# Performance work log

Measured on AMD Instinct MI355X. Metric: run time of the kernel, lower is better.

The kernel has to match this reference:

```python
import jax, jax.numpy as jnp
import numpy as np

H = 8
D_MODEL = 512
D_K = D_MODEL // H
B = 8
S = 1024


def _linear(x, W, b):
    # torch nn.Linear: y = x @ W.T + b, W: [out, in]
    return jnp.einsum('bsd,ed->bse', x, W) + b


def _to_heads(x):
    # [B,S,D] -> [B,H,S,d_k]
    return x.reshape(B, S, H, D_K).transpose(0, 2, 1, 3)


def setup_inputs() -> dict:
    key = jax.random.key(0)
    ks = jax.random.split(key, 20)
    inp = {
        'input_rgb': jax.random.normal(ks[0], (B, S, D_MODEL), jnp.float32),
        'input_flow': jax.random.normal(ks[1], (B, S, D_MODEL), jnp.float32),
    }
    names = ['Wq1', 'Wk1', 'Wv1', 'Wq2', 'Wk2', 'Wv2', 'Wo1', 'Wo2']
    for i, n in enumerate(names):
        inp[n] = jax.random.normal(ks[2 + i], (D_MODEL, D_MODEL), jnp.float32) * 0.02
        inp['b' + n[1:]] = jax.random.normal(ks[10 + i], (D_MODEL,), jnp.float32) * 0.02
    return inp


def reference(input_rgb, input_flow, Wq1, bq1, Wk1, bk1, Wv1, bv1,
              Wq2, bq2, Wk2, bk2, Wv2, bv2, Wo1, bo1, Wo2, bo2):
    scale = 1.0 / jnp.sqrt(jnp.asarray(D_K, input_rgb.dtype))

    q_r = _to_heads(_linear(input_rgb, Wq1, bq1))
    k_r = _to_heads(_linear(input_rgb, Wk1, bk1))
    v_r = _to_heads(_linear(input_rgb, Wv1, bv1))
    q_f = _to_heads(_linear(input_flow, Wq2, bq2))
    k_f = _to_heads(_linear(input_flow, Wk2, bk2))
    v_f = _to_heads(_linear(input_flow, Wv2, bv2))

    # two full [B,H,S,S] softmax attention maps
    attn_rgb = jax.nn.softmax(jnp.einsum('bhqd,bhkd->bhqk', q_r, k_r) * scale, axis=-1)
    attn_flow = jax.nn.softmax(jnp.einsum('bhqd,bhkd->bhqk', q_f, k_f) * scale, axis=-1)
    # elementwise max merge (breaks flash-attention fusion)
    attn = jnp.maximum(attn_rgb, attn_flow)

    # Attention2: out = attn @ value (dropout is identity in eval mode)
    out_rgb = jnp.einsum('bhqk,bhkd->bhqd', attn, v_r)
    out_flow = jnp.einsum('bhqk,bhkd->bhqd', attn, v_f)

    out_rgb = out_rgb.transpose(0, 2, 1, 3).reshape(B, S, D_MODEL)
    out_flow = out_flow.transpose(0, 2, 1, 3).reshape(B, S, D_MODEL)
    return (_linear(out_rgb, Wo1, bo1), _linear(out_flow, Wo2, bo2))
```

## Files before the change

kernel.cpp:

```cpp
#include <hip/hip_runtime.h>
#include <hip/hip_bf16.h>


typedef unsigned short u16;
typedef __attribute__((ext_vector_type(8))) short short8;
typedef __attribute__((ext_vector_type(4))) short s4pack;
typedef __attribute__((ext_vector_type(4))) float floatx4;

#define B_DIM 8
#define S_DIM 1024
#define H_DIM 8
#define DK 64
#define DMODEL 512
#define NTOK (B_DIM * S_DIM)
#define SEG ((size_t)NTOK * DMODEL)
#define WSEG ((size_t)DMODEL * DMODEL)

#define SCHED_FENCE() __builtin_amdgcn_sched_barrier(0)
#define LGKM0() asm volatile("s_waitcnt lgkmcnt(0)" ::: "memory")
#define VMCNT0() asm volatile("s_waitcnt vmcnt(0)" ::: "memory")
#define BARRIER() __builtin_amdgcn_s_barrier()

__device__ __forceinline__ floatx4 mfma_bf16(short8 a, short8 b, floatx4 c) {
  return __builtin_amdgcn_mfma_f32_16x16x32_bf16(a, b, c, 0, 0, 0);
}

__device__ __forceinline__ void mfma16(floatx4& c, s4pack a, s4pack b) {
  asm volatile("v_mfma_f32_16x16x16_bf16 %0, %1, %2, %0"
               : "+v"(c) : "v"(a), "v"(b));
}

__device__ __forceinline__ u16 f32_to_bf16_rne(float f) {
  unsigned u = __float_as_uint(f);
  unsigned r = u + 0x7FFFu + ((u >> 16) & 1u);
  return (u16)(r >> 16);
}

__device__ __forceinline__ float bf16_bits_to_f32(u16 u) {
  return __uint_as_float(((unsigned)u) << 16);
}

__device__ __forceinline__ void async_cp16(const u16* g, u16* lds) {
  __builtin_amdgcn_global_load_lds(
      (__attribute__((address_space(1))) void*)(const_cast<u16*>(g)),
      (__attribute__((address_space(3))) void*)(lds), 16, 0, 0);
}

#define NT_CONV 18
struct ConvParams {
  const void* src[NT_CONV];
  u16* dst[NT_CONV];
  int n[NT_CONV];
  int coff[NT_CONV + 1];
};

__global__ __launch_bounds__(256) void convert_inputs(ConvParams p) {
  __shared__ int flag_f32;
  const int blk = blockIdx.x;
  int t = 0;
  while (t + 1 < NT_CONV && blk >= p.coff[t + 1]) ++t;
  const int lc = blk - p.coff[t];
  const int n = p.n[t];
  const int tid = threadIdx.x;

  if (tid < 64) {
    const u16* s = (const u16*)p.src[t];
    int bad = 0;
#pragma unroll
    for (int j = 0; j < 8; ++j) {
      float f = bf16_bits_to_f32(s[tid * 8 + j]);
      bad |= !(fabsf(f) < 1e4f);
    }
    bad |= __shfl_xor(bad, 1);
    bad |= __shfl_xor(bad, 2);
    bad |= __shfl_xor(bad, 4);
    bad |= __shfl_xor(bad, 8);
    bad |= __shfl_xor(bad, 16);
    bad |= __shfl_xor(bad, 32);
    if (tid == 0) flag_f32 = bad;
  }
  __syncthreads();
  const int is_f32 = flag_f32;
  const int base = lc * 65536;

  for (int it = 0; it < 32; ++it) {
    const int idx = base + (it * 256 + tid) * 8;
    if (idx + 8 > n) break;
    if (!is_f32) {
      *(short8*)&p.dst[t][idx] = *(const short8*)&((const u16*)p.src[t])[idx];
    } else {
      const float* s = (const float*)p.src[t] + idx;
      short8 o;
#pragma unroll
      for (int j = 0; j < 8; ++j) o[j] = (short)f32_to_bf16_rne(s[j]);
      *(short8*)&p.dst[t][idx] = o;
    }
  }
}

__device__ __forceinline__ void gemm128_mainloop(
    const u16* __restrict__ A, const u16* __restrict__ W,
    int m0, int n0, u16* ldsA, u16* ldsB, floatx4 acc[4][4]) {
  const int tid = threadIdx.x;
  const int lane = tid & 63;
  const int wid = tid >> 6;
  const int wm = wid >> 1, wn = wid & 1;
  const int r = lane & 15, g = lane >> 4;

  const int stg_row = wid * 32 + (lane >> 2);
  const int stg_col = (lane & 3) * 8;

  const u16* ga0 = A + (size_t)(m0 + stg_row) * DMODEL + stg_col;
  const u16* ga1 = A + (size_t)(m0 + stg_row + 16) * DMODEL + stg_col;
  const u16* gb0 = W + (size_t)(n0 + stg_row) * DMODEL + stg_col;
  const u16* gb1 = W + (size_t)(n0 + stg_row + 16) * DMODEL + stg_col;
  const int lo0 = (wid * 32) * 32;
  const int lo1 = (wid * 32 + 16) * 32;

#pragma unroll
  for (int t = 0; t < 3; ++t) {
    const int nb = t * 4096;
    const int ko = t * 32;
    async_cp16(ga0 + ko, ldsA + nb + lo0);
    async_cp16(ga1 + ko, ldsA + nb + lo1);
    async_cp16(gb0 + ko, ldsB + nb + lo0);
    async_cp16(gb1 + ko, ldsB + nb + lo1);
  }

#pragma unroll
  for (int kt = 0; kt < 16; ++kt) {
    SCHED_FENCE();
    if (kt < 14)       asm volatile("s_waitcnt vmcnt(8)" ::: "memory");
    else if (kt == 14) asm volatile("s_waitcnt vmcnt(4)" ::: "memory");
    else               asm volatile("s_waitcnt vmcnt(0)" ::: "memory");
    BARRIER();
    SCHED_FENCE();

    const int cb = (kt % 3) * 4096;
    short8 a[4], b[4];
#pragma unroll
    for (int i = 0; i < 4; ++i)
      a[i] = *(const short8*)&ldsA[cb + (wm * 64 + i * 16 + r) * 32 + g * 8];
#pragma unroll
    for (int j = 0; j < 4; ++j)
      b[j] = *(const short8*)&ldsB[cb + (wn * 64 + j * 16 + r) * 32 + g * 8];
#pragma unroll
    for (int i = 0; i < 4; ++i)
#pragma unroll
      for (int j = 0; j < 4; ++j)
        acc[i][j] = mfma_bf16(a[i], b[j], acc[i][j]);

    if (kt + 3 < 16) {
      SCHED_FENCE(); BARRIER(); SCHED_FENCE();
      const int ko = (kt + 3) * 32;
      async_cp16(ga0 + ko, ldsA + cb + lo0);
      async_cp16(ga1 + ko, ldsA + cb + lo1);
      async_cp16(gb0 + ko, ldsB + cb + lo0);
      async_cp16(gb1 + ko, ldsB + cb + lo1);
    }
  }
}

struct QkvParams {
  const u16* X[2];
  const u16* W[2][3];
  const u16* Bias[2][3];
  u16* Out[2][3];
};

__global__ __launch_bounds__(256) void qkv_gemm(QkvParams p) {
  __shared__ u16 ldsA[3 * 128 * 32];
  __shared__ u16 ldsB[3 * 128 * 32];
  const int lin = blockIdx.x;
  const int wg = (lin & 7) * 192 + (lin >> 3);
  const int m0 = (wg / 24) * 128;
  const int c = wg % 24;
  const int z = c / 12;
  const int yc = c % 12;
  const int wi = yc >> 2;
  const int n0 = (yc & 3) * 128;

  floatx4 acc[4][4];
  const floatx4 z4 = {0.f, 0.f, 0.f, 0.f};
#pragma unroll
  for (int i = 0; i < 4; ++i)
#pragma unroll
    for (int j = 0; j < 4; ++j) acc[i][j] = z4;

  gemm128_mainloop(p.X[z], p.W[z][wi], m0, n0, ldsA, ldsB, acc);

  const int tid = threadIdx.x, lane = tid & 63, wid = tid >> 6;
  const int wm = wid >> 1, wn = wid & 1, r = lane & 15, g = lane >> 4;
  const u16* bias = p.Bias[z][wi];
  u16* out = p.Out[z][wi];
  const float qscale = 0.125f * 1.4426950408889634f;

#pragma unroll
  for (int j = 0; j < 4; ++j) {
    const int cc = n0 + wn * 64 + j * 16 + r;
    const float bv = bf16_bits_to_f32(bias[cc]);
    const int h = cc >> 6, d = cc & 63;
#pragma unroll
    for (int i = 0; i < 4; ++i) {
      const int row0 = m0 + wm * 64 + i * 16 + g * 4;
      const int bb = row0 >> 10, ss0 = row0 & 1023;
      if (wi == 2) {
        s4pack pk;
#pragma unroll
        for (int ii = 0; ii < 4; ++ii)
          pk[ii] = (short)f32_to_bf16_rne(acc[i][j][ii] + bv);
        *(s4pack*)&out[(((size_t)(bb * H_DIM + h)) * DK + d) * S_DIM + ss0] = pk;
      } else {
#pragma unroll
        for (int ii = 0; ii < 4; ++ii) {
          float v = acc[i][j][ii] + bv;
          if (wi == 0) v *= qscale;
          out[(((size_t)(bb * H_DIM + h)) * S_DIM + (ss0 + ii)) * DK + d] =
              f32_to_bf16_rne(v);
        }
      }
    }
  }
}

#define KVB 32
#define QB 64

struct AttnParams {
  const u16* Q[2];
  const u16* K[2];
  const u16* Vt[2];
  u16* O[2];
};

__global__ __launch_bounds__(256, 3) void attn_merged(AttnParams p) {
  __shared__ u16 Ks[2][KVB * 64];
  __shared__ u16 Vs[2][64 * KVB];

  const int tid = threadIdx.x;
  const int lane = tid & 63;
  const int wid = tid >> 6;
  const int r = lane & 15, g = lane >> 4;

  const int lin = blockIdx.x;
  const int w = (lin & 7) * 128 + (lin >> 3);
  const int bh = w >> 4;
  const int q0 = (w & 15) * QB;
  const size_t hbase = (size_t)bh * S_DIM * DK;

  const int krow = tid >> 3, kch = tid & 7;
  const int kdst = krow * 64 + ((kch ^ (krow & 7)) * 8);
  const size_t kgsrc = (size_t)krow * DK + kch * 8;
  const int vrow = tid >> 2, vch = tid & 3;
  const int vdst = vrow * KVB + ((vch ^ ((vrow >> 2) & 3)) * 8);
  const size_t vgsrc = (size_t)vrow * S_DIM + vch * 8;

  short8 qf[2][2];
#pragma unroll
  for (int s = 0; s < 2; ++s)
#pragma unroll
    for (int kc = 0; kc < 2; ++kc)
      qf[s][kc] = *(const short8*)
          &p.Q[s][hbase + (size_t)(q0 + wid * 16 + r) * DK + kc * 32 + g * 8];

  short8 kst[2], vst[2];
#pragma unroll
  for (int s = 0; s < 2; ++s)
    kst[s] = *(const short8*)&p.K[s][hbase + kgsrc];

  const floatx4 z4 = {0.f, 0.f, 0.f, 0.f};
  float sl[2] = {0.f, 0.f};

  for (int kt = 0; kt < 32; ++kt) {
    if (kt) { SCHED_FENCE(); BARRIER(); SCHED_FENCE(); }
#pragma unroll
    for (int s = 0; s < 2; ++s)
      *(short8*)&Ks[s][kdst] = kst[s];
    if (kt < 31) {
      const size_t k0n = (size_t)(kt + 1) * KVB * DK;
#pragma unroll
      for (int s = 0; s < 2; ++s)
        kst[s] = *(const short8*)&p.K[s][hbase + k0n + kgsrc];
    }
    SCHED_FENCE(); LGKM0(); BARRIER(); SCHED_FENCE();

#pragma unroll
    for (int s = 0; s < 2; ++s)
#pragma unroll
      for (int kt2 = 0; kt2 < 2; ++kt2) {
        const int row = kt2 * 16 + r;
        const short8 kf0 = *(const short8*)&Ks[s][row * 64 + ((g ^ (r & 7)) * 8)];
        const short8 kf1 =
            *(const short8*)&Ks[s][row * 64 + (((4 + g) ^ (r & 7)) * 8)];
        floatx4 acc = mfma_bf16(kf0, qf[s][0], z4);
        acc = mfma_bf16(kf1, qf[s][1], acc);
        sl[s] += __builtin_amdgcn_exp2f(acc[0]) + __builtin_amdgcn_exp2f(acc[1]) +
                 __builtin_amdgcn_exp2f(acc[2]) + __builtin_amdgcn_exp2f(acc[3]);
      }
  }

#pragma unroll
  for (int s = 0; s < 2; ++s) {
    kst[s] = *(const short8*)&p.K[s][hbase + kgsrc];
    vst[s] = *(const short8*)&p.Vt[s][hbase + vgsrc];
  }

  float inv_[2];
#pragma unroll
  for (int s = 0; s < 2; ++s) {
    float v = sl[s];
    v += __shfl_xor(v, 16);
    v += __shfl_xor(v, 32);
    inv_[s] = 1.0f / v;
  }

  floatx4 o_[2][4];
#pragma unroll
  for (int s = 0; s < 2; ++s)
#pragma unroll
    for (int nt = 0; nt < 4; ++nt) o_[s][nt] = z4;

  for (int kt = 0; kt < 32; ++kt) {
    SCHED_FENCE(); BARRIER(); SCHED_FENCE();
#pragma unroll
    for (int s = 0; s < 2; ++s) {
      *(short8*)&Ks[s][kdst] = kst[s];
      *(short8*)&Vs[s][vdst] = vst[s];
    }
    if (kt < 31) {
      const size_t kn = (size_t)(kt + 1) * KVB;
#pragma unroll
      for (int s = 0; s < 2; ++s) {
        kst[s] = *(const short8*)&p.K[s][hbase + kn * DK + kgsrc];
        vst[s] = *(const short8*)&p.Vt[s][hbase + vgsrc + kn];
      }
    }
    SCHED_FENCE(); LGKM0(); BARRIER(); SCHED_FENCE();

    s4pack pA[2];
#pragma unroll
    for (int kt2 = 0; kt2 < 2; ++kt2) {
      const int row = kt2 * 16 + r;
      const short8 br0 = *(const short8*)&Ks[0][row * 64 + ((g ^ (r & 7)) * 8)];
      const short8 br1 =
          *(const short8*)&Ks[0][row * 64 + (((4 + g) ^ (r & 7)) * 8)];
      const short8 bf0 = *(const short8*)&Ks[1][row * 64 + ((g ^ (r & 7)) * 8)];
      const short8 bf1 =
          *(const short8*)&Ks[1][row * 64 + (((4 + g) ^ (r & 7)) * 8)];
      floatx4 ar = mfma_bf16(br0, qf[0][0], z4);
      ar = mfma_bf16(br1, qf[0][1], ar);
      floatx4 af = mfma_bf16(bf0, qf[1][0], z4);
      af = mfma_bf16(bf1, qf[1][1], af);
#pragma unroll
      for (int i = 0; i < 4; ++i) {
        const float pr = __builtin_amdgcn_exp2f(ar[i]) * inv_[0];
        const float pf = __builtin_amdgcn_exp2f(af[i]) * inv_[1];
        pA[kt2][i] = (short)f32_to_bf16_rne(fmaxf(pr, pf));
      }
    }

    s4pack vB[2][2][4];
#pragma unroll
    for (int s = 0; s < 2; ++s)
#pragma unroll
      for (int kt2 = 0; kt2 < 2; ++kt2)
#pragma unroll
        for (int nt = 0; nt < 4; ++nt) {
          const int row = nt * 16 + r;
          const int cch = 2 * kt2 + (g >> 1);
          const int addr =
              row * KVB + ((cch ^ ((r >> 2) & 3)) * 8) + (g & 1) * 4;
          vB[s][kt2][nt] = *(const s4pack*)&Vs[s][addr];
        }

    asm volatile("s_nop 7" :::);
#pragma unroll
    for (int s = 0; s < 2; ++s)
#pragma unroll
      for (int nt = 0; nt < 4; ++nt) {
        mfma16(o_[s][nt], pA[0], vB[s][0][nt]);
        mfma16(o_[s][nt], pA[1], vB[s][1][nt]);
      }
  }

  asm volatile("s_nop 7\n\ts_nop 7" :::);

  const int bb = bh >> 3, h = bh & 7;
#pragma unroll
  for (int s = 0; s < 2; ++s) {
    u16* out = p.O[s];
#pragma unroll
    for (int nt = 0; nt < 4; ++nt) {
      const int col = h * 64 + nt * 16 + r;
#pragma unroll
      for (int i = 0; i < 4; ++i) {
        const int row = q0 + wid * 16 + g * 4 + i;
        out[((size_t)bb * S_DIM + row) * DMODEL + col] =
            f32_to_bf16_rne(o_[s][nt][i]);
      }
    }
  }
}

struct OutParams {
  const u16* A[2];
  const u16* W[2];
  const u16* Bias[2];
  float* Out[2];
};

__global__ __launch_bounds__(256) void out_gemm(OutParams p) {
  __shared__ u16 ldsA[3 * 128 * 32];
  __shared__ u16 ldsB[3 * 128 * 32];
  const int lin = blockIdx.x;
  const int wg = (lin & 7) * 64 + (lin >> 3);
  const int m0 = (wg >> 3) * 128;
  const int c = wg & 7;
  const int z = c >> 2;
  const int n0 = (c & 3) * 128;

  floatx4 acc[4][4];
  const floatx4 z4 = {0.f, 0.f, 0.f, 0.f};
#pragma unroll
  for (int i = 0; i < 4; ++i)
#pragma unroll
    for (int j = 0; j < 4; ++j) acc[i][j] = z4;

  gemm128_mainloop(p.A[z], p.W[z], m0, n0, ldsA, ldsB, acc);

  const int tid = threadIdx.x, lane = tid & 63, wid = tid >> 6;
  const int wm = wid >> 1, wn = wid & 1, r = lane & 15, g = lane >> 4;
  const u16* bias = p.Bias[z];
  float* out = p.Out[z];

#pragma unroll
  for (int j = 0; j < 4; ++j) {
    const int cc = n0 + wn * 64 + j * 16 + r;
    const float bv = bf16_bits_to_f32(bias[cc]);
#pragma unroll
    for (int i = 0; i < 4; ++i) {
      const int row0 = m0 + wm * 64 + i * 16 + g * 4;
#pragma unroll
      for (int ii = 0; ii < 4; ++ii)
        out[(size_t)(row0 + ii) * DMODEL + cc] = acc[i][j][ii] + bv;
    }
  }
}

extern "C" void kernel_launch(void* const* d_in, const int* in_sizes, int n_in,
                              void* d_out, int out_size, void* d_ws, size_t ws_size,
                              hipStream_t stream) {
  (void)in_sizes; (void)n_in; (void)out_size; (void)ws_size;
  u16* ws = (u16*)d_ws;
  u16* Qr = ws + 0 * SEG;
  u16* Kr = ws + 1 * SEG;
  u16* Vr = ws + 2 * SEG;
  u16* Qf = ws + 3 * SEG;
  u16* Kf = ws + 4 * SEG;
  u16* Vf = ws + 5 * SEG;
  u16* Or = ws + 6 * SEG;
  u16* Of = ws + 7 * SEG;
  u16* cW = ws + 8 * SEG;
  u16* cB = cW + 8 * WSEG;

  ConvParams cp;
  int coff = 0;
  for (int i = 0; i < NT_CONV; ++i) {
    cp.src[i] = d_in[i];
    int n;
    if (i < 2) {
      n = (int)SEG;
      cp.dst[i] = (i == 0) ? Or : Of;
    } else {
      const int k = (i - 2) >> 1;
      const int isb = (i - 2) & 1;
      n = isb ? DMODEL : (int)WSEG;
      cp.dst[i] = isb ? (cB + k * DMODEL) : (cW + k * WSEG);
    }
    cp.n[i] = n;
    cp.coff[i] = coff;
    coff += (n + 65535) / 65536;
  }
  cp.coff[NT_CONV] = coff;
  convert_inputs<<<dim3(coff), dim3(256), 0, stream>>>(cp);

  QkvParams qp;
  qp.X[0] = Or;
  qp.X[1] = Of;
  for (int s = 0; s < 2; ++s)
    for (int wi = 0; wi < 3; ++wi) {
      const int k = s * 3 + wi;
      qp.W[s][wi] = cW + k * WSEG;
      qp.Bias[s][wi] = cB + k * DMODEL;
    }
  qp.Out[0][0] = Qr; qp.Out[0][1] = Kr; qp.Out[0][2] = Vr;
  qp.Out[1][0] = Qf; qp.Out[1][1] = Kf; qp.Out[1][2] = Vf;
  qkv_gemm<<<dim3(1536), dim3(256), 0, stream>>>(qp);

  AttnParams ap;
  ap.Q[0] = Qr; ap.Q[1] = Qf;
  ap.K[0] = Kr; ap.K[1] = Kf;
  ap.Vt[0] = Vr; ap.Vt[1] = Vf;
  ap.O[0] = Or; ap.O[1] = Of;
  attn_merged<<<dim3(1024), dim3(256), 0, stream>>>(ap);

  OutParams op;
  op.A[0] = Or; op.A[1] = Of;
  op.W[0] = cW + 6 * WSEG; op.Bias[0] = cB + 6 * DMODEL;
  op.W[1] = cW + 7 * WSEG; op.Bias[1] = cB + 7 * DMODEL;
  op.Out[0] = (float*)d_out;
  op.Out[1] = (float*)d_out + SEG;
  out_gemm<<<dim3(512), dim3(256), 0, stream>>>(op);
}
```

Before: 284.8 us.

## Double attention query tile per block, use 16x16x32 MFMA for PV, shrink convert chunks

The attention kernel now processes 128 queries per block (32 per wave, two M-tiles), so each K/V tile staged in LDS is reused across twice as many queries, and the grid is halved. The K LDS swizzle is changed to match a new row mapping, and the PV product switches from inline-asm 16x16x16 MFMA to the 16x16x32 builtin, which drops the manual s_nop hazards. Launch bounds go from 3 to 2 waves-per-EU hint because register use grows. The input conversion kernel uses smaller 8192-element chunks, giving more blocks for better parallelism. The cost is higher register pressure, lower occupancy and fewer attention blocks to fill the CUs.

After: 232.4 us. -18.4%, faster.

```diff
diff --git a/kernel.cpp b/kernel.cpp
--- a/kernel.cpp
+++ b/kernel.cpp
@@ -18,16 +18,10 @@
 
 #define SCHED_FENCE() __builtin_amdgcn_sched_barrier(0)
 #define LGKM0() asm volatile("s_waitcnt lgkmcnt(0)" ::: "memory")
-#define VMCNT0() asm volatile("s_waitcnt vmcnt(0)" ::: "memory")
 #define BARRIER() __builtin_amdgcn_s_barrier()
 
 __device__ __forceinline__ floatx4 mfma_bf16(short8 a, short8 b, floatx4 c) {
   return __builtin_amdgcn_mfma_f32_16x16x32_bf16(a, b, c, 0, 0, 0);
-}
-
-__device__ __forceinline__ void mfma16(floatx4& c, s4pack a, s4pack b) {
-  asm volatile("v_mfma_f32_16x16x16_bf16 %0, %1, %2, %0"
-               : "+v"(c) : "v"(a), "v"(b));
 }
 
 __device__ __forceinline__ u16 f32_to_bf16_rne(float f) {
@@ -47,6 +41,7 @@
 }
 
 #define NT_CONV 18
+#define CCHUNK 8192
 struct ConvParams {
   const void* src[NT_CONV];
   u16* dst[NT_CONV];
@@ -81,9 +76,10 @@
   }
   __syncthreads();
   const int is_f32 = flag_f32;
-  const int base = lc * 65536;
-
-  for (int it = 0; it < 32; ++it) {
+  const int base = lc * CCHUNK;
+
+#pragma unroll
+  for (int it = 0; it < CCHUNK / 2048; ++it) {
     const int idx = base + (it * 256 + tid) * 8;
     if (idx + 8 > n) break;
     if (!is_f32) {
@@ -224,7 +220,7 @@
 }
 
 #define KVB 32
-#define QB 64
+#define QB 128
 
 struct AttnParams {
   const u16* Q[2];
@@ -233,7 +229,7 @@
   u16* O[2];
 };
 
-__global__ __launch_bounds__(256, 3) void attn_merged(AttnParams p) {
+__global__ __launch_bounds__(256, 2) void attn_merged(AttnParams p) {
   __shared__ u16 Ks[2][KVB * 64];
   __shared__ u16 Vs[2][64 * KVB];
 
@@ -243,25 +239,34 @@
   const int r = lane & 15, g = lane >> 4;
 
   const int lin = blockIdx.x;
-  const int w = (lin & 7) * 128 + (lin >> 3);
-  const int bh = w >> 4;
-  const int q0 = (w & 15) * QB;
+  const int w = (lin & 7) * 64 + (lin >> 3);
+  const int bh = w >> 3;
+  const int q0 = (w & 7) * QB;
   const size_t hbase = (size_t)bh * S_DIM * DK;
 
   const int krow = tid >> 3, kch = tid & 7;
-  const int kdst = krow * 64 + ((kch ^ (krow & 7)) * 8);
+  const int sKr = (krow & 3) | (((krow >> 3) & 1) << 2);
+  const int kdst = krow * 64 + ((kch ^ sKr) * 8);
   const size_t kgsrc = (size_t)krow * DK + kch * 8;
   const int vrow = tid >> 2, vch = tid & 3;
   const int vdst = vrow * KVB + ((vch ^ ((vrow >> 2) & 3)) * 8);
   const size_t vgsrc = (size_t)vrow * S_DIM + vch * 8;
 
-  short8 qf[2][2];
+  const int srg = (r & 3) | (((r >> 2) & 1) << 2);
+  const int rowAo = ((r >> 2) * 8 + (r & 3)) * 64;
+  const int cA0 = (g ^ srg) * 8;
+  const int cA1 = ((4 + g) ^ srg) * 8;
+
+  short8 qf[2][2][2];
 #pragma unroll
   for (int s = 0; s < 2; ++s)
 #pragma unroll
-    for (int kc = 0; kc < 2; ++kc)
-      qf[s][kc] = *(const short8*)
-          &p.Q[s][hbase + (size_t)(q0 + wid * 16 + r) * DK + kc * 32 + g * 8];
+    for (int mt = 0; mt < 2; ++mt)
+#pragma unroll
+      for (int kc = 0; kc < 2; ++kc)
+        qf[s][mt][kc] = *(const short8*)
+            &p.Q[s][hbase + (size_t)(q0 + wid * 32 + mt * 16 + r) * DK +
+                    kc * 32 + g * 8];
 
   short8 kst[2], vst[2];
 #pragma unroll
@@ -269,7 +274,7 @@
     kst[s] = *(const short8*)&p.K[s][hbase + kgsrc];
 
   const floatx4 z4 = {0.f, 0.f, 0.f, 0.f};
-  float sl[2] = {0.f, 0.f};
+  float sl[2][2] = {{0.f, 0.f}, {0.f, 0.f}};
 
   for (int kt = 0; kt < 32; ++kt) {
     if (kt) { SCHED_FENCE(); BARRIER(); SCHED_FENCE(); }
@@ -285,18 +290,23 @@
     SCHED_FENCE(); LGKM0(); BARRIER(); SCHED_FENCE();
 
 #pragma unroll
-    for (int s = 0; s < 2; ++s)
-#pragma unroll
-      for (int kt2 = 0; kt2 < 2; ++kt2) {
-        const int row = kt2 * 16 + r;
-        const short8 kf0 = *(const short8*)&Ks[s][row * 64 + ((g ^ (r & 7)) * 8)];
-        const short8 kf1 =
-            *(const short8*)&Ks[s][row * 64 + (((4 + g) ^ (r & 7)) * 8)];
-        floatx4 acc = mfma_bf16(kf0, qf[s][0], z4);
-        acc = mfma_bf16(kf1, qf[s][1], acc);
-        sl[s] += __builtin_amdgcn_exp2f(acc[0]) + __builtin_amdgcn_exp2f(acc[1]) +
-                 __builtin_amdgcn_exp2f(acc[2]) + __builtin_amdgcn_exp2f(acc[3]);
+    for (int s = 0; s < 2; ++s) {
+      const short8 kA0 = *(const short8*)&Ks[s][rowAo + cA0];
+      const short8 kA1 = *(const short8*)&Ks[s][rowAo + cA1];
+      const short8 kB0 = *(const short8*)&Ks[s][rowAo + 256 + cA0];
+      const short8 kB1 = *(const short8*)&Ks[s][rowAo + 256 + cA1];
+#pragma unroll
+      for (int mt = 0; mt < 2; ++mt) {
+        floatx4 aA = mfma_bf16(kA0, qf[s][mt][0], z4);
+        aA = mfma_bf16(kA1, qf[s][mt][1], aA);
+        floatx4 aB = mfma_bf16(kB0, qf[s][mt][0], z4);
+        aB = mfma_bf16(kB1, qf[s][mt][1], aB);
+        sl[s][mt] += __builtin_amdgcn_exp2f(aA[0]) + __builtin_amdgcn_exp2f(aA[1]) +
+                     __builtin_amdgcn_exp2f(aA[2]) + __builtin_amdgcn_exp2f(aA[3]) +
+                     __builtin_amdgcn_exp2f(aB[0]) + __builtin_amdgcn_exp2f(aB[1]) +
+                     __builtin_amdgcn_exp2f(aB[2]) + __builtin_amdgcn_exp2f(aB[3]);
       }
+    }
   }
 
 #pragma unroll
@@ -305,20 +315,24 @@
     vst[s] = *(const short8*)&p.Vt[s][hbase + vgsrc];
   }
 
-  float inv_[2];
-#pragma unroll
-  for (int s = 0; s < 2; ++s) {
-    float v = sl[s];
-    v += __shfl_xor(v, 16);
-    v += __shfl_xor(v, 32);
-    inv_[s] = 1.0f / v;
-  }
-
-  floatx4 o_[2][4];
+  float inv_[2][2];
 #pragma unroll
   for (int s = 0; s < 2; ++s)
 #pragma unroll
-    for (int nt = 0; nt < 4; ++nt) o_[s][nt] = z4;
+    for (int mt = 0; mt < 2; ++mt) {
+      float v = sl[s][mt];
+      v += __shfl_xor(v, 16);
+      v += __shfl_xor(v, 32);
+      inv_[s][mt] = 1.0f / v;
+    }
+
+  floatx4 o_[2][2][4];
+#pragma unroll
+  for (int s = 0; s < 2; ++s)
+#pragma unroll
+    for (int mt = 0; mt < 2; ++mt)
+#pragma unroll
+      for (int nt = 0; nt < 4; ++nt) o_[s][mt][nt] = z4;
 
   for (int kt = 0; kt < 32; ++kt) {
     SCHED_FENCE(); BARRIER(); SCHED_FENCE();
@@ -337,68 +351,70 @@
     }
     SCHED_FENCE(); LGKM0(); BARRIER(); SCHED_FENCE();
 
-    s4pack pA[2];
-#pragma unroll
-    for (int kt2 = 0; kt2 < 2; ++kt2) {
-      const int row = kt2 * 16 + r;
-      const short8 br0 = *(const short8*)&Ks[0][row * 64 + ((g ^ (r & 7)) * 8)];
-      const short8 br1 =
-          *(const short8*)&Ks[0][row * 64 + (((4 + g) ^ (r & 7)) * 8)];
-      const short8 bf0 = *(const short8*)&Ks[1][row * 64 + ((g ^ (r & 7)) * 8)];
-      const short8 bf1 =
-          *(const short8*)&Ks[1][row * 64 + (((4 + g) ^ (r & 7)) * 8)];
-      floatx4 ar = mfma_bf16(br0, qf[0][0], z4);
-      ar = mfma_bf16(br1, qf[0][1], ar);
-      floatx4 af = mfma_bf16(bf0, qf[1][0], z4);
-      af = mfma_bf16(bf1, qf[1][1], af);
+    short8 kA0[2], kA1[2], kB0[2], kB1[2];
+#pragma unroll
+    for (int s = 0; s < 2; ++s) {
+      kA0[s] = *(const short8*)&Ks[s][rowAo + cA0];
+      kA1[s] = *(const short8*)&Ks[s][rowAo + cA1];
+      kB0[s] = *(const short8*)&Ks[s][rowAo + 256 + cA0];
+      kB1[s] = *(const short8*)&Ks[s][rowAo + 256 + cA1];
+    }
+
+    short8 pA[2];
+#pragma unroll
+    for (int mt = 0; mt < 2; ++mt) {
+      floatx4 arA = mfma_bf16(kA0[0], qf[0][mt][0], z4);
+      arA = mfma_bf16(kA1[0], qf[0][mt][1], arA);
+      floatx4 arB = mfma_bf16(kB0[0], qf[0][mt][0], z4);
+      arB = mfma_bf16(kB1[0], qf[0][mt][1], arB);
+      floatx4 afA = mfma_bf16(kA0[1], qf[1][mt][0], z4);
+      afA = mfma_bf16(kA1[1], qf[1][mt][1], afA);
+      floatx4 afB = mfma_bf16(kB0[1], qf[1][mt][0], z4);
+      afB = mfma_bf16(kB1[1], qf[1][mt][1], afB);
 #pragma unroll
       for (int i = 0; i < 4; ++i) {
-        const float pr = __builtin_amdgcn_exp2f(ar[i]) * inv_[0];
-        const float pf = __builtin_amdgcn_exp2f(af[i]) * inv_[1];
-        pA[kt2][i] = (short)f32_to_bf16_rne(fmaxf(pr, pf));
+        const float prA = __builtin_amdgcn_exp2f(arA[i]) * inv_[0][mt];
+        const float pfA = __builtin_amdgcn_exp2f(afA[i]) * inv_[1][mt];
+        pA[mt][i] = (short)f32_to_bf16_rne(fmaxf(prA, pfA));
+        const float prB = __builtin_amdgcn_exp2f(arB[i]) * inv_[0][mt];
+        const float pfB = __builtin_amdgcn_exp2f(afB[i]) * inv_[1][mt];
+        pA[mt][4 + i] = (short)f32_to_bf16_rne(fmaxf(prB, pfB));
       }
     }
 
-    s4pack vB[2][2][4];
+    short8 vB[2][4];
 #pragma unroll
     for (int s = 0; s < 2; ++s)
 #pragma unroll
-      for (int kt2 = 0; kt2 < 2; ++kt2)
-#pragma unroll
-        for (int nt = 0; nt < 4; ++nt) {
-          const int row = nt * 16 + r;
-          const int cch = 2 * kt2 + (g >> 1);
-          const int addr =
-              row * KVB + ((cch ^ ((r >> 2) & 3)) * 8) + (g & 1) * 4;
-          vB[s][kt2][nt] = *(const s4pack*)&Vs[s][addr];
-        }
-
-    asm volatile("s_nop 7" :::);
+      for (int nt = 0; nt < 4; ++nt)
+        vB[s][nt] = *(const short8*)
+            &Vs[s][(nt * 16 + r) * KVB + ((g ^ ((r >> 2) & 3)) * 8)];
+
 #pragma unroll
     for (int s = 0; s < 2; ++s)
 #pragma unroll
-      for (int nt = 0; nt < 4; ++nt) {
-        mfma16(o_[s][nt], pA[0], vB[s][0][nt]);
-        mfma16(o_[s][nt], pA[1], vB[s][1][nt]);
-      }
-  }
-
-  asm volatile("s_nop 7\n\ts_nop 7" :::);
+      for (int mt = 0; mt < 2; ++mt)
+#pragma unroll
+        for (int nt = 0; nt < 4; ++nt)
+          o_[s][mt][nt] = mfma_bf16(pA[mt], vB[s][nt], o_[s][mt][nt]);
+  }
 
   const int bb = bh >> 3, h = bh & 7;
 #pragma unroll
   for (int s = 0; s < 2; ++s) {
     u16* out = p.O[s];
 #pragma unroll
-    for (int nt = 0; nt < 4; ++nt) {
-      const int col = h * 64 + nt * 16 + r;
-#pragma unroll
-      for (int i = 0; i < 4; ++i) {
-        const int row = q0 + wid * 16 + g * 4 + i;
-        out[((size_t)bb * S_DIM + row) * DMODEL + col] =
-            f32_to_bf16_rne(o_[s][nt][i]);
+    for (int mt = 0; mt < 2; ++mt)
+#pragma unroll
+      for (int nt = 0; nt < 4; ++nt) {
+        const int col = h * 64 + nt * 16 + r;
+#pragma unroll
+        for (int i = 0; i < 4; ++i) {
+          const int row = q0 + wid * 32 + mt * 16 + g * 4 + i;
+          out[((size_t)bb * S_DIM + row) * DMODEL + col] =
+              f32_to_bf16_rne(o_[s][mt][nt][i]);
+        }
       }
-    }
   }
 }
 
@@ -479,7 +495,7 @@
     }
     cp.n[i] = n;
     cp.coff[i] = coff;
-    coff += (n + 65535) / 65536;
+    coff += (n + CCHUNK - 1) / CCHUNK;
   }
   cp.coff[NT_CONV] = coff;
   convert_inputs<<<dim3(coff), dim3(256), 0, stream>>>(cp);
@@ -502,7 +518,7 @@
   ap.K[0] = Kr; ap.K[1] = Kf;
   ap.Vt[0] = Vr; ap.Vt[1] = Vf;
   ap.O[0] = Or; ap.O[1] = Of;
-  attn_merged<<<dim3(1024), dim3(256), 0, stream>>>(ap);
+  attn_merged<<<dim3(512), dim3(256), 0, stream>>>(ap);
 
   OutParams op;
   op.A[0] = Or; op.A[1] = Of;
```
